# Kernel tuning notes

Measured on AMD Instinct MI355X. Metric: run time of the kernel, lower is better.

## Reference

```python
import jax, jax.numpy as jnp
import numpy as np

NHEAD = 16
D_MODEL = 1024
D_K = D_MODEL // NHEAD


def setup_inputs() -> dict:
    key = jax.random.key(0)
    ks = jax.random.split(key, 12)
    B, S, D = 2, 2048, D_MODEL
    scale = 1.0 / np.sqrt(D)
    inp = {
        "value": jax.random.normal(ks[0], (B, S, D), dtype=jnp.float32),
        "key": jax.random.normal(ks[1], (B, S, D), dtype=jnp.float32),
        "query": jax.random.normal(ks[2], (B, S, D), dtype=jnp.float32),
        "mask": jax.random.randint(ks[3], (B, 1, S, S), 0, 2, dtype=jnp.int32),
        "Wv": jax.random.normal(ks[4], (D, D), dtype=jnp.float32) * scale,
        "bv": jnp.zeros((D,), dtype=jnp.float32),
        "Wk": jax.random.normal(ks[5], (D, D), dtype=jnp.float32) * scale,
        "bk": jnp.zeros((D,), dtype=jnp.float32),
        "Wq": jax.random.normal(ks[6], (D, D), dtype=jnp.float32) * scale,
        "bq": jnp.zeros((D,), dtype=jnp.float32),
        "Wo": jax.random.normal(ks[7], (D, D), dtype=jnp.float32) * scale,
        "bo": jnp.zeros((D,), dtype=jnp.float32),
    }
    return inp


def reference(value, key, query, mask, Wv, bv, Wk, bk, Wq, bq, Wo, bo):
    B, S, D = value.shape
    H, Dk = NHEAD, D_K

    def proj(x, W, b):
        # nn.Linear: x @ W^T + b, then split heads -> [B, H, S, Dk]
        return (x @ W.T + b).reshape(B, S, H, Dk).transpose(0, 2, 1, 3)

    v = proj(value, Wv, bv)
    k = proj(key, Wk, bk)
    q = proj(query, Wq, bq)

    # NOTE: source code swaps K and V when calling attention():
    #   scores = Q @ V^T / sqrt(d_k);  out = softmax(scores) @ K
    scores = jnp.einsum("bhqd,bhkd->bhqk", q, v) / jnp.sqrt(jnp.float32(Dk))
    scores = jnp.where(mask == 0, jnp.float32(-1e9), scores)
    attn = jax.nn.softmax(scores, axis=-1)  # [B, H, S, S]
    attr_value = jnp.einsum("bhqk,bhkd->bhqd", attn, k)

    out = attr_value.transpose(0, 2, 1, 3).reshape(B, S, H * Dk)
    return out @ Wo.T + bo
```

## Files before the change

kernel.cpp:

```cpp
#include <hip/hip_runtime.h>

#define S_LEN 2048
#define DMODEL 1024
#define NHEADS 16
#define DKH 64

typedef __attribute__((ext_vector_type(8))) short bf16x8;
typedef __attribute__((ext_vector_type(4))) float f32x4;

static __device__ __forceinline__ short f2bf(float f) {
    unsigned b = __float_as_uint(f);
    b = (b + 0x7FFFu + ((b >> 16) & 1u)) >> 16;
    return (short)b;
}

static __device__ __forceinline__ f32x4 mfma16(bf16x8 a, bf16x8 b, f32x4 c) {
    return __builtin_amdgcn_mfma_f32_16x16x32_bf16(a, b, c, 0, 0, 0);
}

static __device__ __forceinline__ void glds16(const short* g, short* l) {
    __builtin_amdgcn_global_load_lds(
        (const __attribute__((address_space(1))) void*)g,
        (__attribute__((address_space(3))) void*)l, 16, 0, 0);
}

struct CvtArgs { const float* src[7]; short* dst[7]; };

__global__ __launch_bounds__(256) void cvt_bf16(CvtArgs a) {
    const size_t i8 = ((size_t)blockIdx.x * 256 + threadIdx.x) * 8;
    int seg; size_t off;
    if (i8 < ((size_t)12 << 20)) { seg = (int)(i8 >> 22); off = i8 & ((1u << 22) - 1); }
    else { size_t r = i8 - ((size_t)12 << 20); seg = 3 + (int)(r >> 20); off = r & ((1u << 20) - 1); }
    const float* s = a.src[seg] + off;
    float4 x0 = *(const float4*)s, x1 = *(const float4*)(s + 4);
    short o[8];
    o[0] = f2bf(x0.x); o[1] = f2bf(x0.y); o[2] = f2bf(x0.z); o[3] = f2bf(x0.w);
    o[4] = f2bf(x1.x); o[5] = f2bf(x1.y); o[6] = f2bf(x1.z); o[7] = f2bf(x1.w);
    *(uint4*)(a.dst[seg] + off) = *(uint4*)o;
}

__global__ __launch_bounds__(256) void pack_mask(const int* __restrict__ mask,
                                                 unsigned long long* __restrict__ mw) {
    const int wave = (blockIdx.x << 2) + (threadIdx.x >> 6);
    const int lane = threadIdx.x & 63;
    const size_t base = (size_t)wave * 64;
    for (int it = 0; it < 64; ++it) {
        const size_t w = base + it;
        const int m = mask[(w << 6) + lane];
        unsigned long long bal = __ballot(m != 0);
        if (lane == 0) mw[w] = bal;
    }
}

struct GemmArgs { const short* X[3]; const short* W[3]; const float* B[3]; void* C[3]; };

template <int MODE>
__global__ __launch_bounds__(256) void gemm_bt(GemmArgs a) {
    __shared__ short Ah[128 * 32];
    __shared__ short Bh[128 * 32];
    const int z = blockIdx.z;
    const short* X = a.X[z];
    const short* W = a.W[z];
    const float* bias = a.B[z];

    const int t = threadIdx.x, wid = t >> 6, lane = t & 63;
    const int l15 = lane & 15, lq = lane >> 4;
    const int m0 = blockIdx.x << 7, n0 = blockIdx.y << 7;
    const int wm = (wid >> 1) << 6, wn = (wid & 1) << 6;

    const int kb = (lane & 3) ^ ((lane >> 3) & 3);
    const int r0 = (wid << 5) + (lane >> 2);
    const short* ag0 = X + (size_t)(m0 + r0) * 1024 + (kb << 3);
    const short* ag1 = ag0 + 16 * 1024;
    const short* bg0 = W + (size_t)(n0 + r0) * 1024 + (kb << 3);
    const short* bg1 = bg0 + 16 * 1024;
    short* lA0 = Ah + (wid << 5) * 32;
    short* lA1 = lA0 + 16 * 32;
    short* lB0 = Bh + (wid << 5) * 32;
    short* lB1 = lB0 + 16 * 32;

    const int fpos = (lq ^ ((l15 >> 1) & 3)) << 3;

    f32x4 acc[4][4] = {};

    for (int k0 = 0; k0 < 1024; k0 += 32) {
        __syncthreads();
        glds16(ag0, lA0); glds16(ag1, lA1);
        glds16(bg0, lB0); glds16(bg1, lB1);
        ag0 += 32; ag1 += 32; bg0 += 32; bg1 += 32;
        __syncthreads();

        bf16x8 af[4], bfr[4];
        #pragma unroll
        for (int i = 0; i < 4; ++i)
            af[i] = *(const bf16x8*)&Ah[(wm + i * 16 + l15) * 32 + fpos];
        #pragma unroll
        for (int j = 0; j < 4; ++j)
            bfr[j] = *(const bf16x8*)&Bh[(wn + j * 16 + l15) * 32 + fpos];
        #pragma unroll
        for (int i = 0; i < 4; ++i)
            #pragma unroll
            for (int j = 0; j < 4; ++j)
                acc[i][j] = mfma16(af[i], bfr[j], acc[i][j]);
    }

    #pragma unroll
    for (int j = 0; j < 4; ++j) {
        const int n = n0 + wn + j * 16 + l15;
        const float bn = bias[n];
        #pragma unroll
        for (int i = 0; i < 4; ++i) {
            const int mbase = m0 + wm + i * 16 + (lq << 2);
            #pragma unroll
            for (int r = 0; r < 4; ++r) {
                const float val = acc[i][j][r] + bn;
                const int m = mbase + r;
                if (MODE == 0) {
                    const int b = m >> 11, s = m & 2047, h = n >> 6, d = n & 63;
                    ((short*)a.C[z])[((((size_t)(b * 16 + h)) << 11) + s) * 64 + d] = f2bf(val);
                } else {
                    ((float*)a.C[z])[((size_t)m << 10) + n] = val;
                }
            }
        }
    }
}

__global__ __launch_bounds__(256) void attn_mfma(
    const short* __restrict__ Qh, const short* __restrict__ Vh,
    const short* __restrict__ Kh, const unsigned long long* __restrict__ MW,
    short* __restrict__ attr)
{
    constexpr int VP = 72;
    __shared__ short Vs[64 * VP];
    __shared__ short Kt[64 * VP];
    __shared__ short Ps[128 * VP];

    const int t = threadIdx.x, wid = t >> 6, lane = t & 63;
    const int l15 = lane & 15, lq = lane >> 4;
    const int bh = blockIdx.y, b = bh >> 4, h = bh & 15;
    const int q0 = blockIdx.x << 7;

    bf16x8 qf[2][2];
    #pragma unroll
    for (int mt = 0; mt < 2; ++mt) {
        const short* qp = Qh + ((size_t)bh * 2048 + q0 + (wid << 5) + mt * 16 + l15) * 64 + (lq << 3);
        qf[mt][0] = *(const bf16x8*)qp;
        qf[mt][1] = *(const bf16x8*)(qp + 32);
    }

    const int vrow = t >> 2, vcb = (t & 3) << 4;
    const int kj = lane, kdb = wid << 4;
    const int kphi = ((kj & 15) << 2) + (kj >> 4);

    const short* vg = Vh + (size_t)bh * 2048 * 64;
    const short* kg = Kh + (size_t)bh * 2048 * 64;
    const unsigned long long* mwp = MW + ((size_t)b * 2048 + q0 + (wid << 5) + (lq << 2)) * 32;

    float rsum[2][4] = {};
    f32x4 O[2][4] = {};

    for (int jc = 0; jc < 32; ++jc) {
        const int j0 = jc << 6;
        __syncthreads();
        {
            const short* p = vg + (size_t)(j0 + vrow) * 64 + vcb;
            *(uint4*)&Vs[vrow * VP + vcb + 0] = *(const uint4*)p;
            *(uint4*)&Vs[vrow * VP + vcb + 8] = *(const uint4*)(p + 8);
        }
        {
            const short* p = kg + (size_t)(j0 + kj) * 64 + kdb;
            short kv[16];
            *(uint4*)(kv + 0) = *(const uint4*)(p + 0);
            *(uint4*)(kv + 8) = *(const uint4*)(p + 8);
            #pragma unroll
            for (int e = 0; e < 16; ++e)
                Kt[(kdb + e) * VP + kphi] = kv[e];
        }
        uint2 mwv[2][4];
        #pragma unroll
        for (int mt = 0; mt < 2; ++mt)
            #pragma unroll
            for (int r = 0; r < 4; ++r)
                mwv[mt][r] = *(const uint2*)&mwp[(size_t)(mt * 16 + r) * 32 + jc];
        __syncthreads();

        bf16x8 vf[4][2];
        #pragma unroll
        for (int nt = 0; nt < 4; ++nt) {
            vf[nt][0] = *(const bf16x8*)&Vs[(nt * 16 + l15) * VP + (lq << 3)];
            vf[nt][1] = *(const bf16x8*)&Vs[(nt * 16 + l15) * VP + 32 + (lq << 3)];
        }

        #pragma unroll
        for (int mt = 0; mt < 2; ++mt) {
            f32x4 sc[4];
            #pragma unroll
            for (int nt = 0; nt < 4; ++nt) {
                f32x4 c = {};
                c = mfma16(qf[mt][0], vf[nt][0], c);
                c = mfma16(qf[mt][1], vf[nt][1], c);
                sc[nt] = c;
            }
            #pragma unroll
            for (int r = 0; r < 4; ++r) {
                ushort4 pb;
                #pragma unroll
                for (int nt = 0; nt < 4; ++nt) {
                    const unsigned sel = (nt < 2) ? mwv[mt][r].x : mwv[mt][r].y;
                    const unsigned bit = (sel >> ((nt & 1) * 16 + l15)) & 1u;
                    float p = __expf(sc[nt][r] * 0.125f);
                    p = bit ? p : 0.f;
                    const unsigned u = __float_as_uint(p) & 0xFFFF0000u;
                    rsum[mt][r] += __uint_as_float(u);
                    ((unsigned short*)&pb)[nt] = (unsigned short)(u >> 16);
                }
                *(ushort4*)&Ps[((wid << 5) + mt * 16 + (lq << 2) + r) * VP + (l15 << 2)] = pb;
            }
        }

        bf16x8 pf[2][2];
        #pragma unroll
        for (int mt = 0; mt < 2; ++mt) {
            const short* pp = &Ps[((wid << 5) + mt * 16 + l15) * VP];
            pf[mt][0] = *(const bf16x8*)(pp + (lq << 3));
            pf[mt][1] = *(const bf16x8*)(pp + 32 + (lq << 3));
        }
        #pragma unroll
        for (int nt = 0; nt < 4; ++nt) {
            const short* kp = &Kt[(nt * 16 + l15) * VP];
            bf16x8 kf0 = *(const bf16x8*)(kp + (lq << 3));
            bf16x8 kf1 = *(const bf16x8*)(kp + 32 + (lq << 3));
            #pragma unroll
            for (int mt = 0; mt < 2; ++mt) {
                O[mt][nt] = mfma16(pf[mt][0], kf0, O[mt][nt]);
                O[mt][nt] = mfma16(pf[mt][1], kf1, O[mt][nt]);
            }
        }
    }

    #pragma unroll
    for (int mt = 0; mt < 2; ++mt)
        #pragma unroll
        for (int r = 0; r < 4; ++r) {
            float s = rsum[mt][r];
            #pragma unroll
            for (int d = 1; d < 16; d <<= 1)
                s += __shfl_xor(s, d, 64);
            rsum[mt][r] = s;
        }

    #pragma unroll
    for (int mt = 0; mt < 2; ++mt)
        #pragma unroll
        for (int r = 0; r < 4; ++r) {
            const float inv = 1.f / rsum[mt][r];
            const size_t row = (size_t)b * 2048 + q0 + (wid << 5) + mt * 16 + (lq << 2) + r;
            #pragma unroll
            for (int nt = 0; nt < 4; ++nt)
                attr[row * 1024 + (h << 6) + nt * 16 + l15] = f2bf(O[mt][nt][r] * inv);
        }
}

extern "C" void kernel_launch(void* const* d_in, const int* in_sizes, int n_in,
                              void* d_out, int out_size, void* d_ws, size_t ws_size,
                              hipStream_t stream) {
    const float* value = (const float*)d_in[0];
    const float* key   = (const float*)d_in[1];
    const float* query = (const float*)d_in[2];
    const int*   mask  = (const int*)d_in[3];
    const float* bv = (const float*)d_in[5];
    const float* bk = (const float*)d_in[7];
    const float* bq = (const float*)d_in[9];
    const float* bo = (const float*)d_in[11];
    float* out = (float*)d_out;

    const size_t M1 = (size_t)1 << 20, M4 = (size_t)1 << 22;
    short* ws = (short*)d_ws;
    short* Xq = ws;
    short* Xk = ws + M4;
    short* Xv = ws + 2 * M4;
    short* Wc0 = ws + 3 * M4;
    short* Wc1 = Wc0 + M1;
    short* Wc2 = Wc1 + M1;
    short* Wc3 = Wc2 + M1;
    short* qh = ws + 4 * M4;
    short* kh = ws + 5 * M4;
    short* vh = ws + 6 * M4;
    unsigned long long* maskw = (unsigned long long*)(ws + 7 * M4);
    short* attr = Xq;

    CvtArgs cv;
    cv.src[0] = query; cv.dst[0] = Xq;
    cv.src[1] = key;   cv.dst[1] = Xk;
    cv.src[2] = value; cv.dst[2] = Xv;
    cv.src[3] = (const float*)d_in[8];  cv.dst[3] = Wc0;
    cv.src[4] = (const float*)d_in[6];  cv.dst[4] = Wc1;
    cv.src[5] = (const float*)d_in[4];  cv.dst[5] = Wc2;
    cv.src[6] = (const float*)d_in[10]; cv.dst[6] = Wc3;
    cvt_bf16<<<8192, 256, 0, stream>>>(cv);

    pack_mask<<<512, 256, 0, stream>>>(mask, maskw);

    GemmArgs g1;
    g1.X[0] = Xq; g1.W[0] = Wc0; g1.B[0] = bq; g1.C[0] = qh;
    g1.X[1] = Xk; g1.W[1] = Wc1; g1.B[1] = bk; g1.C[1] = kh;
    g1.X[2] = Xv; g1.W[2] = Wc2; g1.B[2] = bv; g1.C[2] = vh;
    gemm_bt<0><<<dim3(32, 8, 3), 256, 0, stream>>>(g1);

    attn_mfma<<<dim3(16, 32), 256, 0, stream>>>(qh, vh, kh, maskw, attr);

    GemmArgs g2;
    g2.X[0] = attr; g2.W[0] = Wc3; g2.B[0] = bo; g2.C[0] = out;
    g2.X[1] = attr; g2.W[1] = Wc3; g2.B[1] = bo; g2.C[1] = out;
    g2.X[2] = attr; g2.W[2] = Wc3; g2.B[2] = bo; g2.C[2] = out;
    gemm_bt<1><<<dim3(32, 8, 1), 256, 0, stream>>>(g2);
}
```

Measured before the change: 315.3 us.

## Pre-transpose K, drop LDS staging in attention, fold softmax scale into Q projection

Adds a separate kernel that writes K transposed, with the key-position permutation baked in, so the attention kernel loads V and K MFMA fragments directly from global memory. This removes the shared-memory staging of V and K and both per-iteration block barriers. The 1/sqrt(dk)*log2(e) factor is folded into the Q projection epilogue so softmax uses a raw exp2. The convert and mask-pack kernels are merged into one launch. The cost is an extra transpose pass over K and uncoalesced, redundant global fragment loads that now depend on L2 instead of LDS.

```diff
diff --git a/kernel.cpp b/kernel.cpp
--- a/kernel.cpp
+++ b/kernel.cpp
@@ -8,6 +8,14 @@
 typedef __attribute__((ext_vector_type(8))) short bf16x8;
 typedef __attribute__((ext_vector_type(4))) float f32x4;
 
+#if __has_builtin(__builtin_amdgcn_exp2f)
+#define EXP2F(x) __builtin_amdgcn_exp2f(x)
+#define QSCALE (0.125f * 1.44269504f)
+#else
+#define EXP2F(x) __expf(x)
+#define QSCALE 0.125f
+#endif
+
 static __device__ __forceinline__ short f2bf(float f) {
     unsigned b = __float_as_uint(f);
     b = (b + 0x7FFFu + ((b >> 16) & 1u)) >> 16;
@@ -26,33 +34,35 @@
 
 struct CvtArgs { const float* src[7]; short* dst[7]; };
 
-__global__ __launch_bounds__(256) void cvt_bf16(CvtArgs a) {
-    const size_t i8 = ((size_t)blockIdx.x * 256 + threadIdx.x) * 8;
-    int seg; size_t off;
-    if (i8 < ((size_t)12 << 20)) { seg = (int)(i8 >> 22); off = i8 & ((1u << 22) - 1); }
-    else { size_t r = i8 - ((size_t)12 << 20); seg = 3 + (int)(r >> 20); off = r & ((1u << 20) - 1); }
-    const float* s = a.src[seg] + off;
-    float4 x0 = *(const float4*)s, x1 = *(const float4*)(s + 4);
-    short o[8];
-    o[0] = f2bf(x0.x); o[1] = f2bf(x0.y); o[2] = f2bf(x0.z); o[3] = f2bf(x0.w);
-    o[4] = f2bf(x1.x); o[5] = f2bf(x1.y); o[6] = f2bf(x1.z); o[7] = f2bf(x1.w);
-    *(uint4*)(a.dst[seg] + off) = *(uint4*)o;
-}
-
-__global__ __launch_bounds__(256) void pack_mask(const int* __restrict__ mask,
-                                                 unsigned long long* __restrict__ mw) {
-    const int wave = (blockIdx.x << 2) + (threadIdx.x >> 6);
-    const int lane = threadIdx.x & 63;
-    const size_t base = (size_t)wave * 64;
-    for (int it = 0; it < 64; ++it) {
-        const size_t w = base + it;
-        const int m = mask[(w << 6) + lane];
-        unsigned long long bal = __ballot(m != 0);
-        if (lane == 0) mw[w] = bal;
-    }
-}
-
-struct GemmArgs { const short* X[3]; const short* W[3]; const float* B[3]; void* C[3]; };
+__global__ __launch_bounds__(256) void prep(CvtArgs a, const int* __restrict__ mask,
+                                            unsigned long long* __restrict__ mw) {
+    if (blockIdx.x < 8192) {
+        const size_t i8 = ((size_t)blockIdx.x * 256 + threadIdx.x) * 8;
+        int seg; size_t off;
+        if (i8 < ((size_t)12 << 20)) { seg = (int)(i8 >> 22); off = i8 & ((1u << 22) - 1); }
+        else { size_t r = i8 - ((size_t)12 << 20); seg = 3 + (int)(r >> 20); off = r & ((1u << 20) - 1); }
+        const float* s = a.src[seg] + off;
+        float4 x0 = *(const float4*)s, x1 = *(const float4*)(s + 4);
+        short o[8];
+        o[0] = f2bf(x0.x); o[1] = f2bf(x0.y); o[2] = f2bf(x0.z); o[3] = f2bf(x0.w);
+        o[4] = f2bf(x1.x); o[5] = f2bf(x1.y); o[6] = f2bf(x1.z); o[7] = f2bf(x1.w);
+        *(uint4*)(a.dst[seg] + off) = *(uint4*)o;
+    } else {
+        const int wv = ((blockIdx.x - 8192) << 2) + (threadIdx.x >> 6);
+        const int lane = threadIdx.x & 63;
+        const size_t base = (size_t)wv << 4;
+        #pragma unroll 4
+        for (int it = 0; it < 16; ++it) {
+            const size_t w = base + it;
+            const int m = mask[(w << 6) + lane];
+            unsigned long long bal = __ballot(m != 0);
+            if (lane == 0) mw[w] = bal;
+        }
+    }
+}
+
+struct GemmArgs { const short* X[3]; const short* W[3]; const float* B[3];
+                  void* C[3]; float scale[3]; };
 
 template <int MODE>
 __global__ __launch_bounds__(256) void gemm_bt(GemmArgs a) {
@@ -62,6 +72,7 @@
     const short* X = a.X[z];
     const short* W = a.W[z];
     const float* bias = a.B[z];
+    const float scl = a.scale[z];
 
     const int t = threadIdx.x, wid = t >> 6, lane = t & 63;
     const int l15 = lane & 15, lq = lane >> 4;
@@ -113,7 +124,7 @@
             const int mbase = m0 + wm + i * 16 + (lq << 2);
             #pragma unroll
             for (int r = 0; r < 4; ++r) {
-                const float val = acc[i][j][r] + bn;
+                const float val = (acc[i][j][r] + bn) * scl;
                 const int m = mbase + r;
                 if (MODE == 0) {
                     const int b = m >> 11, s = m & 2047, h = n >> 6, d = n & 63;
@@ -126,71 +137,79 @@
     }
 }
 
-__global__ __launch_bounds__(256) void attn_mfma(
+__global__ __launch_bounds__(256) void ktr(const short* __restrict__ kh,
+                                           short* __restrict__ kt) {
+    __shared__ short Ls[64 * 68];
+    const int t = threadIdx.x;
+    const int s0 = blockIdx.x << 6, bh = blockIdx.y;
+    {
+        const int r = t >> 2, cb = (t & 3) << 4;
+        const short* src = kh + ((size_t)bh * 2048 + s0 + r) * 64 + cb;
+        *(uint4*)&Ls[r * 68 + cb + 0] = *(const uint4*)src;
+        *(uint4*)&Ls[r * 68 + cb + 8] = *(const uint4*)(src + 8);
+    }
+    __syncthreads();
+    const int d = t >> 2, c0 = (t & 3) << 4;
+    short ov[16];
+    #pragma unroll
+    for (int e = 0; e < 16; ++e) {
+        const int c = c0 + e;
+        const int jl = ((c & 3) << 4) | (c >> 2);
+        ov[e] = Ls[jl * 68 + d];
+    }
+    short* dst = kt + ((size_t)bh * 64 + d) * 2048 + s0 + c0;
+    *(uint4*)(dst + 0) = *(uint4*)(ov + 0);
+    *(uint4*)(dst + 8) = *(uint4*)(ov + 8);
+}
+
+__global__ __launch_bounds__(256) void attn2(
     const short* __restrict__ Qh, const short* __restrict__ Vh,
-    const short* __restrict__ Kh, const unsigned long long* __restrict__ MW,
+    const short* __restrict__ Kt, const unsigned long long* __restrict__ MW,
     short* __restrict__ attr)
 {
-    constexpr int VP = 72;
-    __shared__ short Vs[64 * VP];
-    __shared__ short Kt[64 * VP];
+    constexpr int VP = 68;
     __shared__ short Ps[128 * VP];
 
     const int t = threadIdx.x, wid = t >> 6, lane = t & 63;
     const int l15 = lane & 15, lq = lane >> 4;
     const int bh = blockIdx.y, b = bh >> 4, h = bh & 15;
     const int q0 = blockIdx.x << 7;
+    const int rowbase = q0 + (wid << 5);
 
     bf16x8 qf[2][2];
     #pragma unroll
     for (int mt = 0; mt < 2; ++mt) {
-        const short* qp = Qh + ((size_t)bh * 2048 + q0 + (wid << 5) + mt * 16 + l15) * 64 + (lq << 3);
+        const short* qp = Qh + ((size_t)bh * 2048 + rowbase + mt * 16 + l15) * 64 + (lq << 3);
         qf[mt][0] = *(const bf16x8*)qp;
         qf[mt][1] = *(const bf16x8*)(qp + 32);
     }
 
-    const int vrow = t >> 2, vcb = (t & 3) << 4;
-    const int kj = lane, kdb = wid << 4;
-    const int kphi = ((kj & 15) << 2) + (kj >> 4);
-
-    const short* vg = Vh + (size_t)bh * 2048 * 64;
-    const short* kg = Kh + (size_t)bh * 2048 * 64;
-    const unsigned long long* mwp = MW + ((size_t)b * 2048 + q0 + (wid << 5) + (lq << 2)) * 32;
+    const short* vgb = Vh + (size_t)bh * 2048 * 64;
+    const short* kgb = Kt + (size_t)bh * 64 * 2048;
+    const unsigned long long* mwp = MW + ((size_t)b * 2048 + rowbase) * 32;
 
     float rsum[2][4] = {};
     f32x4 O[2][4] = {};
 
     for (int jc = 0; jc < 32; ++jc) {
         const int j0 = jc << 6;
-        __syncthreads();
-        {
-            const short* p = vg + (size_t)(j0 + vrow) * 64 + vcb;
-            *(uint4*)&Vs[vrow * VP + vcb + 0] = *(const uint4*)p;
-            *(uint4*)&Vs[vrow * VP + vcb + 8] = *(const uint4*)(p + 8);
-        }
-        {
-            const short* p = kg + (size_t)(j0 + kj) * 64 + kdb;
-            short kv[16];
-            *(uint4*)(kv + 0) = *(const uint4*)(p + 0);
-            *(uint4*)(kv + 8) = *(const uint4*)(p + 8);
-            #pragma unroll
-            for (int e = 0; e < 16; ++e)
-                Kt[(kdb + e) * VP + kphi] = kv[e];
+
+        bf16x8 vf[4][2], kf[4][2];
+        #pragma unroll
+        for (int nt = 0; nt < 4; ++nt) {
+            const short* vp = vgb + (size_t)(j0 + nt * 16 + l15) * 64 + (lq << 3);
+            vf[nt][0] = *(const bf16x8*)vp;
+            vf[nt][1] = *(const bf16x8*)(vp + 32);
+            const short* kp = kgb + (size_t)(nt * 16 + l15) * 2048 + j0 + (lq << 3);
+            kf[nt][0] = *(const bf16x8*)kp;
+            kf[nt][1] = *(const bf16x8*)(kp + 32);
         }
         uint2 mwv[2][4];
         #pragma unroll
         for (int mt = 0; mt < 2; ++mt)
             #pragma unroll
             for (int r = 0; r < 4; ++r)
-                mwv[mt][r] = *(const uint2*)&mwp[(size_t)(mt * 16 + r) * 32 + jc];
-        __syncthreads();
-
-        bf16x8 vf[4][2];
-        #pragma unroll
-        for (int nt = 0; nt < 4; ++nt) {
-            vf[nt][0] = *(const bf16x8*)&Vs[(nt * 16 + l15) * VP + (lq << 3)];
-            vf[nt][1] = *(const bf16x8*)&Vs[(nt * 16 + l15) * VP + 32 + (lq << 3)];
-        }
+                mwv[mt][r] = *(const uint2*)&mwp[(size_t)(mt * 16 + (lq << 2) + r) * 32 + jc];
 
         #pragma unroll
         for (int mt = 0; mt < 2; ++mt) {
@@ -204,18 +223,20 @@
             }
             #pragma unroll
             for (int r = 0; r < 4; ++r) {
-                ushort4 pb;
+                unsigned px0 = 0, px1 = 0;
                 #pragma unroll
                 for (int nt = 0; nt < 4; ++nt) {
                     const unsigned sel = (nt < 2) ? mwv[mt][r].x : mwv[mt][r].y;
-                    const unsigned bit = (sel >> ((nt & 1) * 16 + l15)) & 1u;
-                    float p = __expf(sc[nt][r] * 0.125f);
+                    const unsigned bit = (sel >> (((nt & 1) << 4) + l15)) & 1u;
+                    float p = EXP2F(sc[nt][r]);
                     p = bit ? p : 0.f;
                     const unsigned u = __float_as_uint(p) & 0xFFFF0000u;
                     rsum[mt][r] += __uint_as_float(u);
-                    ((unsigned short*)&pb)[nt] = (unsigned short)(u >> 16);
+                    if (nt & 1) { if (nt >> 1) px1 |= u; else px0 |= u; }
+                    else        { if (nt >> 1) px1 = u >> 16; else px0 = u >> 16; }
                 }
-                *(ushort4*)&Ps[((wid << 5) + mt * 16 + (lq << 2) + r) * VP + (l15 << 2)] = pb;
+                uint2 pw; pw.x = px0; pw.y = px1;
+                *(uint2*)&Ps[((wid << 5) + mt * 16 + (lq << 2) + r) * VP + (l15 << 2)] = pw;
             }
         }
 
@@ -227,16 +248,12 @@
             pf[mt][1] = *(const bf16x8*)(pp + 32 + (lq << 3));
         }
         #pragma unroll
-        for (int nt = 0; nt < 4; ++nt) {
-            const short* kp = &Kt[(nt * 16 + l15) * VP];
-            bf16x8 kf0 = *(const bf16x8*)(kp + (lq << 3));
-            bf16x8 kf1 = *(const bf16x8*)(kp + 32 + (lq << 3));
+        for (int nt = 0; nt < 4; ++nt)
             #pragma unroll
             for (int mt = 0; mt < 2; ++mt) {
-                O[mt][nt] = mfma16(pf[mt][0], kf0, O[mt][nt]);
-                O[mt][nt] = mfma16(pf[mt][1], kf1, O[mt][nt]);
+                O[mt][nt] = mfma16(pf[mt][0], kf[nt][0], O[mt][nt]);
+                O[mt][nt] = mfma16(pf[mt][1], kf[nt][1], O[mt][nt]);
             }
-        }
     }
 
     #pragma unroll
@@ -247,15 +264,8 @@
             #pragma unroll
             for (int d = 1; d < 16; d <<= 1)
                 s += __shfl_xor(s, d, 64);
-            rsum[mt][r] = s;
-        }
-
-    #pragma unroll
-    for (int mt = 0; mt < 2; ++mt)
-        #pragma unroll
-        for (int r = 0; r < 4; ++r) {
-            const float inv = 1.f / rsum[mt][r];
-            const size_t row = (size_t)b * 2048 + q0 + (wid << 5) + mt * 16 + (lq << 2) + r;
+            const float inv = 1.f / s;
+            const size_t row = (size_t)b * 2048 + rowbase + mt * 16 + (lq << 2) + r;
             #pragma unroll
             for (int nt = 0; nt < 4; ++nt)
                 attr[row * 1024 + (h << 6) + nt * 16 + l15] = f2bf(O[mt][nt][r] * inv);
@@ -287,7 +297,8 @@
     short* qh = ws + 4 * M4;
     short* kh = ws + 5 * M4;
     short* vh = ws + 6 * M4;
-    unsigned long long* maskw = (unsigned long long*)(ws + 7 * M4);
+    short* kt = ws + 7 * M4;
+    unsigned long long* maskw = (unsigned long long*)(ws + 8 * M4);
     short* attr = Xq;
 
     CvtArgs cv;
@@ -298,21 +309,21 @@
     cv.src[4] = (const float*)d_in[6];  cv.dst[4] = Wc1;
     cv.src[5] = (const float*)d_in[4];  cv.dst[5] = Wc2;
     cv.src[6] = (const float*)d_in[10]; cv.dst[6] = Wc3;
-    cvt_bf16<<<8192, 256, 0, stream>>>(cv);
-
-    pack_mask<<<512, 256, 0, stream>>>(mask, maskw);
+    prep<<<10240, 256, 0, stream>>>(cv, mask, maskw);
 
     GemmArgs g1;
-    g1.X[0] = Xq; g1.W[0] = Wc0; g1.B[0] = bq; g1.C[0] = qh;
-    g1.X[1] = Xk; g1.W[1] = Wc1; g1.B[1] = bk; g1.C[1] = kh;
-    g1.X[2] = Xv; g1.W[2] = Wc2; g1.B[2] = bv; g1.C[2] = vh;
+    g1.X[0] = Xq; g1.W[0] = Wc0; g1.B[0] = bq; g1.C[0] = qh; g1.scale[0] = QSCALE;
+    g1.X[1] = Xk; g1.W[1] = Wc1; g1.B[1] = bk; g1.C[1] = kh; g1.scale[1] = 1.f;
+    g1.X[2] = Xv; g1.W[2] = Wc2; g1.B[2] = bv; g1.C[2] = vh; g1.scale[2] = 1.f;
     gemm_bt<0><<<dim3(32, 8, 3), 256, 0, stream>>>(g1);
 
-    attn_mfma<<<dim3(16, 32), 256, 0, stream>>>(qh, vh, kh, maskw, attr);
+    ktr<<<dim3(32, 32), 256, 0, stream>>>(kh, kt);
+
+    attn2<<<dim3(16, 32), 256, 0, stream>>>(qh, vh, kt, maskw, attr);
 
     GemmArgs g2;
-    g2.X[0] = attr; g2.W[0] = Wc3; g2.B[0] = bo; g2.C[0] = out;
-    g2.X[1] = attr; g2.W[1] = Wc3; g2.B[1] = bo; g2.C[1] = out;
-    g2.X[2] = attr; g2.W[2] = Wc3; g2.B[2] = bo; g2.C[2] = out;
+    g2.X[0] = attr; g2.W[0] = Wc3; g2.B[0] = bo; g2.C[0] = out; g2.scale[0] = 1.f;
+    g2.X[1] = attr; g2.W[1] = Wc3; g2.B[1] = bo; g2.C[1] = out; g2.scale[1] = 1.f;
+    g2.X[2] = attr; g2.W[2] = Wc3; g2.B[2] = bo; g2.C[2] = out; g2.scale[2] = 1.f;
     gemm_bt<1><<<dim3(32, 8, 1), 256, 0, stream>>>(g2);
 }
```

Result: slower. 340.4 us (+8.0%).
